# Kernel tuning notes

Measured on AMD Instinct MI355X. Metric: run time of the kernel, lower is better.

The kernel has to match this reference:

```python
import jax, jax.numpy as jnp
import numpy as np

B, L, H, HEADS, E, MPD = 4, 1024, 768, 12, 22, 128  # batch, seq, hidden, heads, entities/doc, mentions/doc
EMB = 512
M = B * MPD
NE = B * E


def setup_inputs() -> dict:
    key = jax.random.key(0)
    k1, k2, k3, k4, k5 = jax.random.split(key, 5)
    sequence_output = jax.random.normal(k1, (B, L, H), jnp.float32)
    # attention rows are softmax-normalized like real transformer attention
    attention = jax.nn.softmax(jax.random.normal(k2, (B, HEADS, L, L), jnp.float32), axis=-1)
    mention_batch = jnp.repeat(jnp.arange(B, dtype=jnp.int32), MPD)
    mention_pos = jax.random.randint(k3, (M,), 0, L, jnp.int32)
    local = jax.random.randint(k4, (M,), 0, E, jnp.int32)
    # guarantee every entity has >=1 mention (first E mentions of each doc cover 0..E-1)
    within = jnp.arange(M, dtype=jnp.int32) % MPD
    local = jnp.where(within < E, within, local)
    mention_entity = mention_batch * E + local
    w_trans = jax.random.normal(k5, (H, EMB), jnp.float32) * 0.02
    b_trans = jnp.zeros((EMB,), jnp.float32)
    return {
        "sequence_output": sequence_output,
        "attention": attention,
        "w_trans": w_trans,
        "b_trans": b_trans,
        "mention_batch": mention_batch,
        "mention_pos": mention_pos,
        "mention_entity": mention_entity,
    }


def reference(sequence_output, attention, w_trans, b_trans,
              mention_batch, mention_pos, mention_entity):
    # --- gather mention reps / attention rows (make_graph inner loop, vectorized) ---
    m_emb = sequence_output[mention_batch, mention_pos]          # [M, H]
    m_att = attention[mention_batch, :, mention_pos, :]          # [M, HEADS, L]

    counts = jax.ops.segment_sum(jnp.ones((M,), jnp.float32), mention_entity,
                                 num_segments=NE)                # [NE]
    has = counts > 0

    # entity embedding = logsumexp over that entity's mentions (stable segment version)
    mx = jax.ops.segment_max(m_emb, mention_entity, num_segments=NE)
    mx = jnp.where(has[:, None], mx, 0.0)
    sums = jax.ops.segment_sum(jnp.exp(m_emb - mx[mention_entity]), mention_entity,
                               num_segments=NE)
    entity_emb = jnp.where(has[:, None], jnp.log(sums + 1e-30) + mx, 0.0)  # [NE, H]

    # entity attention = mean over mentions, then mean over heads, then L1-normalize
    e_att = jax.ops.segment_sum(m_att, mention_entity, num_segments=NE)
    e_att = e_att / (counts[:, None, None] + 1e-5)               # [NE, HEADS, L]
    e_att = e_att.mean(axis=1)                                   # [NE, L]
    e_att = e_att / (e_att.sum(axis=1, keepdims=True) + 1e-5)

    # context pooling: e_context = e_att @ sequence_output (relation_map einsum)
    e_att_b = e_att.reshape(B, E, L)
    e_context = jnp.einsum("bel,blh->beh", e_att_b, sequence_output)  # [B, E, H]

    e_cg = e_context + entity_emb.reshape(B, E, H)
    out = jnp.tanh(e_cg @ w_trans + b_trans)                     # [B, E, EMB]
    return out
```

## Files before the change

kernel.cpp:

```cpp
#include <hip/hip_runtime.h>
#include <hip/hip_bf16.h>
#include <float.h>

#define B 4
#define L 1024
#define H 768
#define HEADS 12
#define E 22
#define MPD 128
#define EMB 512
#define M (B*MPD)
#define NE (B*E)
#define LCH_A 4
#define LCH_B 16
#define LB (L/LCH_B)

__global__ __launch_bounds__(256) void k_gather(
    const float* __restrict__ seq, const float* __restrict__ att,
    const int* __restrict__ m_batch, const int* __restrict__ m_pos,
    const int* __restrict__ m_ent,
    float* __restrict__ e_att_raw, float* __restrict__ e_cg,
    float* __restrict__ zpart, float* __restrict__ cntf)
{
    const int bx = blockIdx.x;
    const int t  = threadIdx.x;
    __shared__ int s_cnt;
    __shared__ size_t s_off[MPD];
    __shared__ float s_p[4];
    if (t == 0) s_cnt = 0;
    __syncthreads();

    if (bx < NE * LCH_A) {
        const int e = bx >> 2, chunk = bx & 3;
        for (int m = t; m < M; m += 256)
            if (m_ent[m] == e) {
                int p = atomicAdd(&s_cnt, 1);
                s_off[p] = (size_t)m_batch[m] * HEADS * L * L + (size_t)m_pos[m] * L;
            }
        __syncthreads();
        const int cnt = s_cnt;
        const int l = chunk * 256 + t;
        float acc = 0.f;
        for (int i = 0; i < cnt; ++i) {
            const float* p = att + s_off[i] + l;
            #pragma unroll
            for (int hd = 0; hd < HEADS; ++hd)
                acc += p[(size_t)hd * L * L];
        }
        e_att_raw[(size_t)e * L + l] = acc;
        float v = acc;
        #pragma unroll
        for (int off = 32; off > 0; off >>= 1) v += __shfl_xor(v, off, 64);
        if ((t & 63) == 0) s_p[t >> 6] = v;
        __syncthreads();
        if (t == 0) {
            zpart[bx] = s_p[0] + s_p[1] + s_p[2] + s_p[3];
            if (chunk == 0) cntf[e] = (float)cnt;
        }
    } else {
        const int e = bx - NE * LCH_A;
        for (int m = t; m < M; m += 256)
            if (m_ent[m] == e) {
                int p = atomicAdd(&s_cnt, 1);
                s_off[p] = ((size_t)m_batch[m] * L + m_pos[m]) * H;
            }
        __syncthreads();
        const int cnt = s_cnt;
        float mx0 = -FLT_MAX, mx1 = -FLT_MAX, mx2 = -FLT_MAX;
        for (int i = 0; i < cnt; ++i) {
            const float* r = seq + s_off[i];
            mx0 = fmaxf(mx0, r[t]);
            mx1 = fmaxf(mx1, r[t + 256]);
            mx2 = fmaxf(mx2, r[t + 512]);
        }
        float s0 = 0.f, s1 = 0.f, s2 = 0.f;
        for (int i = 0; i < cnt; ++i) {
            const float* r = seq + s_off[i];
            s0 += expf(r[t]       - mx0);
            s1 += expf(r[t + 256] - mx1);
            s2 += expf(r[t + 512] - mx2);
        }
        float o0, o1, o2;
        if (cnt > 0) {
            o0 = logf(s0 + 1e-30f) + mx0;
            o1 = logf(s1 + 1e-30f) + mx1;
            o2 = logf(s2 + 1e-30f) + mx2;
        } else { o0 = o1 = o2 = 0.f; }
        float* dst = e_cg + (size_t)e * H;
        dst[t] = o0; dst[t + 256] = o1; dst[t + 512] = o2;
    }
}

__global__ __launch_bounds__(128) void k_context(
    const float* __restrict__ seq, const float* __restrict__ e_att_raw,
    const float* __restrict__ zpart, const float* __restrict__ cntf,
    float* __restrict__ e_cg)
{
    const int ht = blockIdx.x;
    const int lc = blockIdx.y;
    const int b  = blockIdx.z;
    const int t  = threadIdx.x;
    const int h  = ht * 128 + t;
    const int l0 = lc * LB;
    __shared__ float s_att[E][LB];
    __shared__ float s_norm[E];
    for (int i = t; i < E * LB; i += 128) {
        int el = i / LB, dl = i % LB;
        s_att[el][dl] = e_att_raw[(size_t)(b * E + el) * L + l0 + dl];
    }
    if (t < E) {
        int ge = b * E + t;
        float z = zpart[ge * LCH_A] + zpart[ge * LCH_A + 1]
                + zpart[ge * LCH_A + 2] + zpart[ge * LCH_A + 3];
        float c2 = (cntf[ge] + 1e-5f) * (float)HEADS;
        s_norm[t] = 1.f / (z + 1e-5f * c2);
    }
    __syncthreads();
    float acc[E];
    #pragma unroll
    for (int e = 0; e < E; ++e) acc[e] = 0.f;
    const float* sp = seq + ((size_t)b * L + l0) * H + h;
    #pragma unroll 4
    for (int dl = 0; dl < LB; ++dl) {
        float s = sp[(size_t)dl * H];
        #pragma unroll
        for (int e = 0; e < E; ++e) acc[e] += s_att[e][dl] * s;
    }
    float* dst = e_cg + (size_t)(b * E) * H + h;
    #pragma unroll
    for (int e = 0; e < E; ++e) atomicAdd(dst + (size_t)e * H, acc[e] * s_norm[e]);
}

__global__ __launch_bounds__(128) void k_out(
    const float* __restrict__ e_cg, const float* __restrict__ w,
    const float* __restrict__ bias, float* __restrict__ out)
{
    const int row = blockIdx.x;
    const int c   = blockIdx.y * 128 + threadIdx.x;
    __shared__ float s_row[H];
    for (int i = threadIdx.x; i < H; i += 128) s_row[i] = e_cg[(size_t)row * H + i];
    __syncthreads();
    float acc = bias[c];
    #pragma unroll 8
    for (int h = 0; h < H; ++h)
        acc += s_row[h] * w[(size_t)h * EMB + c];
    out[(size_t)row * EMB + c] = tanhf(acc);
}

extern "C" void kernel_launch(void* const* d_in, const int* in_sizes, int n_in,
                              void* d_out, int out_size, void* d_ws, size_t ws_size,
                              hipStream_t stream) {
    const float* seq   = (const float*)d_in[0];
    const float* att   = (const float*)d_in[1];
    const float* w     = (const float*)d_in[2];
    const float* bias  = (const float*)d_in[3];
    const int* m_batch = (const int*)d_in[4];
    const int* m_pos   = (const int*)d_in[5];
    const int* m_ent   = (const int*)d_in[6];
    float* out = (float*)d_out;

    float* ws        = (float*)d_ws;
    float* e_att_raw = ws;
    float* e_cg      = ws + (size_t)NE * L;
    float* zpart     = e_cg + (size_t)NE * H;
    float* cntf      = zpart + NE * LCH_A;

    k_gather<<<NE * LCH_A + NE, 256, 0, stream>>>(
        seq, att, m_batch, m_pos, m_ent, e_att_raw, e_cg, zpart, cntf);
    dim3 gB(H / 128, LCH_B, B);
    k_context<<<gB, 128, 0, stream>>>(seq, e_att_raw, zpart, cntf, e_cg);
    dim3 gC(NE, EMB / 128);
    k_out<<<gC, 128, 0, stream>>>(e_cg, w, bias, out);
}
```

Before: 320.0 us.

## Replace context atomics with per-chunk partial buffers reduced in output kernel

The context kernel now writes per-L-chunk partial sums to a workspace buffer instead of issuing float atomicAdds into the entity rows. The output kernel sums the 16 partials, applies the attention normalization and adds the entity embedding while staging each row in shared memory. The context kernel also loads float2 so each thread covers two hidden columns, which halves the grid and doubles register accumulators. This removes atomic contention and makes the result deterministic. In exchange it adds an extra global partial buffer, the reduction work is repeated in every output block, and register pressure rises.

```diff
diff --git a/kernel.cpp b/kernel.cpp
--- a/kernel.cpp
+++ b/kernel.cpp
@@ -19,7 +19,7 @@
     const float* __restrict__ seq, const float* __restrict__ att,
     const int* __restrict__ m_batch, const int* __restrict__ m_pos,
     const int* __restrict__ m_ent,
-    float* __restrict__ e_att_raw, float* __restrict__ e_cg,
+    float* __restrict__ e_att_raw, float* __restrict__ entity_emb,
     float* __restrict__ zpart, float* __restrict__ cntf)
 {
     const int bx = blockIdx.x;
@@ -86,59 +86,66 @@
             o1 = logf(s1 + 1e-30f) + mx1;
             o2 = logf(s2 + 1e-30f) + mx2;
         } else { o0 = o1 = o2 = 0.f; }
-        float* dst = e_cg + (size_t)e * H;
+        float* dst = entity_emb + (size_t)e * H;
         dst[t] = o0; dst[t + 256] = o1; dst[t + 512] = o2;
     }
 }
 
 __global__ __launch_bounds__(128) void k_context(
     const float* __restrict__ seq, const float* __restrict__ e_att_raw,
-    const float* __restrict__ zpart, const float* __restrict__ cntf,
-    float* __restrict__ e_cg)
+    float* __restrict__ ctx_part)
 {
     const int ht = blockIdx.x;
     const int lc = blockIdx.y;
     const int b  = blockIdx.z;
     const int t  = threadIdx.x;
-    const int h  = ht * 128 + t;
+    const int h  = ht * 256 + t * 2;
     const int l0 = lc * LB;
     __shared__ float s_att[E][LB];
-    __shared__ float s_norm[E];
     for (int i = t; i < E * LB; i += 128) {
         int el = i / LB, dl = i % LB;
         s_att[el][dl] = e_att_raw[(size_t)(b * E + el) * L + l0 + dl];
     }
-    if (t < E) {
-        int ge = b * E + t;
-        float z = zpart[ge * LCH_A] + zpart[ge * LCH_A + 1]
-                + zpart[ge * LCH_A + 2] + zpart[ge * LCH_A + 3];
-        float c2 = (cntf[ge] + 1e-5f) * (float)HEADS;
-        s_norm[t] = 1.f / (z + 1e-5f * c2);
-    }
     __syncthreads();
-    float acc[E];
+    float ax[E], ay[E];
     #pragma unroll
-    for (int e = 0; e < E; ++e) acc[e] = 0.f;
+    for (int e = 0; e < E; ++e) { ax[e] = 0.f; ay[e] = 0.f; }
     const float* sp = seq + ((size_t)b * L + l0) * H + h;
     #pragma unroll 4
     for (int dl = 0; dl < LB; ++dl) {
-        float s = sp[(size_t)dl * H];
+        const float2 s = *(const float2*)(sp + (size_t)dl * H);
         #pragma unroll
-        for (int e = 0; e < E; ++e) acc[e] += s_att[e][dl] * s;
+        for (int e = 0; e < E; ++e) {
+            ax[e] += s_att[e][dl] * s.x;
+            ay[e] += s_att[e][dl] * s.y;
+        }
     }
-    float* dst = e_cg + (size_t)(b * E) * H + h;
     #pragma unroll
-    for (int e = 0; e < E; ++e) atomicAdd(dst + (size_t)e * H, acc[e] * s_norm[e]);
+    for (int e = 0; e < E; ++e) {
+        float2 v; v.x = ax[e]; v.y = ay[e];
+        *(float2*)&ctx_part[((size_t)lc * NE + b * E + e) * H + h] = v;
+    }
 }
 
 __global__ __launch_bounds__(128) void k_out(
-    const float* __restrict__ e_cg, const float* __restrict__ w,
-    const float* __restrict__ bias, float* __restrict__ out)
+    const float* __restrict__ ctx_part, const float* __restrict__ entity_emb,
+    const float* __restrict__ zpart, const float* __restrict__ cntf,
+    const float* __restrict__ w, const float* __restrict__ bias,
+    float* __restrict__ out)
 {
     const int row = blockIdx.x;
     const int c   = blockIdx.y * 128 + threadIdx.x;
     __shared__ float s_row[H];
-    for (int i = threadIdx.x; i < H; i += 128) s_row[i] = e_cg[(size_t)row * H + i];
+    const float z = zpart[row * LCH_A] + zpart[row * LCH_A + 1]
+                  + zpart[row * LCH_A + 2] + zpart[row * LCH_A + 3];
+    const float norm = 1.f / (z + 1e-5f * ((cntf[row] + 1e-5f) * (float)HEADS));
+    for (int h = threadIdx.x; h < H; h += 128) {
+        float sum = 0.f;
+        #pragma unroll
+        for (int lc = 0; lc < LCH_B; ++lc)
+            sum += ctx_part[((size_t)lc * NE + row) * H + h];
+        s_row[h] = sum * norm + entity_emb[(size_t)row * H + h];
+    }
     __syncthreads();
     float acc = bias[c];
     #pragma unroll 8
@@ -159,16 +166,17 @@
     const int* m_ent   = (const int*)d_in[6];
     float* out = (float*)d_out;
 
-    float* ws        = (float*)d_ws;
-    float* e_att_raw = ws;
-    float* e_cg      = ws + (size_t)NE * L;
-    float* zpart     = e_cg + (size_t)NE * H;
-    float* cntf      = zpart + NE * LCH_A;
+    float* ws         = (float*)d_ws;
+    float* e_att_raw  = ws;
+    float* entity_emb = e_att_raw + (size_t)NE * L;
+    float* zpart      = entity_emb + (size_t)NE * H;
+    float* cntf       = zpart + NE * LCH_A;
+    float* ctx_part   = cntf + NE;
 
     k_gather<<<NE * LCH_A + NE, 256, 0, stream>>>(
-        seq, att, m_batch, m_pos, m_ent, e_att_raw, e_cg, zpart, cntf);
-    dim3 gB(H / 128, LCH_B, B);
-    k_context<<<gB, 128, 0, stream>>>(seq, e_att_raw, zpart, cntf, e_cg);
+        seq, att, m_batch, m_pos, m_ent, e_att_raw, entity_emb, zpart, cntf);
+    dim3 gB(H / 256, LCH_B, B);
+    k_context<<<gB, 128, 0, stream>>>(seq, e_att_raw, ctx_part);
     dim3 gC(NE, EMB / 128);
-    k_out<<<gC, 128, 0, stream>>>(e_cg, w, bias, out);
+    k_out<<<gC, 128, 0, stream>>>(ctx_part, entity_emb, zpart, cntf, w, bias, out);
 }
```

Result: no change. 324.3 us (+1.3%).
